# Optimization experiments

Measured on AMD Instinct MI355X. Metric: run time of the kernel, lower is better.

## Reference

```python
import jax, jax.numpy as jnp
import numpy as np
from jax import lax

AB = 2            # activation quant bits (args.ab)
BN_EPS = 1e-4


def binarize(w):
    # DoReFa 1-bit weight: sign(w) with straight-through estimator
    wb = jnp.where(w >= 0, 1.0, -1.0).astype(w.dtype)
    return w + lax.stop_gradient(wb - w)


def quantize(x, bits):
    # uniform quantization of x in [0,1] to `bits` bits, STE backward
    n = float(2 ** bits - 1)
    q = jnp.round(x * n) / n
    return x + lax.stop_gradient(q - x)


def conv(x, w, pad, b=None):
    y = lax.conv_general_dilated(x, w, window_strides=(1, 1),
                                 padding=[(pad, pad), (pad, pad)],
                                 dimension_numbers=('NCHW', 'OIHW', 'NCHW'))
    if b is not None:
        y = y + b[None, :, None, None]
    return y


def maxpool2(x):
    return lax.reduce_window(x, -jnp.inf, lax.max, (1, 1, 2, 2), (1, 1, 2, 2), 'VALID')


def bn(x, gamma, beta, mean, var):
    inv = gamma * lax.rsqrt(var + BN_EPS)
    return (x - mean[None, :, None, None]) * inv[None, :, None, None] + beta[None, :, None, None]


def setup_inputs() -> dict:
    key = jax.random.key(0)
    ks = jax.random.split(key, 16)
    s = lambda k, shape, sc=0.1: jax.random.normal(k, shape, dtype=jnp.float32) * sc
    return {
        'x': jax.random.uniform(ks[0], (4096, 1, 28, 28), dtype=jnp.float32),
        'w1': s(ks[1], (64, 1, 3, 3)), 'b1': s(ks[2], (64,)),
        'w2': s(ks[3], (64, 64, 3, 3)),
        'g1': 1.0 + s(ks[4], (64,)), 'be1': s(ks[5], (64,)),
        'm1': s(ks[6], (64,)), 'v1': 0.5 + jax.random.uniform(ks[7], (64,), dtype=jnp.float32),
        'w3': s(ks[8], (64, 64, 3, 3)),
        'g2': 1.0 + s(ks[9], (64,)), 'be2': s(ks[10], (64,)),
        'm2': s(ks[11], (64,)), 'v2': 0.5 + jax.random.uniform(ks[12], (64,), dtype=jnp.float32),
        'fw1': s(ks[13], (512, 1600)), 'fb1': s(ks[13], (512,)),
        'fw2': s(ks[14], (10, 512)), 'fb2': s(ks[15], (10,)),
    }


def reference(x, w1, b1, w2, g1, be1, m1, v1, w3, g2, be2, m2, v2, fw1, fb1, fw2, fb2):
    x = x.reshape(-1, 1, 28, 28)
    # features
    h = conv(x, binarize(w1), pad=1, b=b1)                 # [B,64,28,28]
    h = maxpool2(h)                                        # [B,64,14,14]
    h = quantize(jnp.clip(h, 0.0, 1.0), AB)
    h = conv(h, binarize(w2), pad=1)                       # [B,64,14,14]
    h = bn(h, g1, be1, m1, v1)
    h = quantize(jnp.clip(h, 0.0, 1.0), AB)
    h = maxpool2(h)                                        # [B,64,7,7]
    h = conv(h, binarize(w3), pad=0)                       # [B,64,5,5]
    h = bn(h, g2, be2, m2, v2)
    h = quantize(jnp.clip(h, 0.0, 1.0), AB)
    # NCHW -> NHWC -> flatten (matches permute((0,2,3,1)) + view)
    h = jnp.transpose(h, (0, 2, 3, 1)).reshape(-1, 64 * 5 * 5)
    # classifier
    h = h @ binarize(fw1).T + fb1                          # [B,512]
    h = h @ fw2.T + fb2                                    # [B,10]
    return jax.nn.log_softmax(h, axis=-1)
```

## Files before the change

kernel.cpp:

```cpp
#include <hip/hip_runtime.h>

#define DEV __device__ __forceinline__

typedef int v4i __attribute__((ext_vector_type(4)));
typedef short v8s __attribute__((ext_vector_type(8)));
typedef float v4f __attribute__((ext_vector_type(4)));
typedef unsigned long long u64;

DEV unsigned int quant3(float y3) {
    return (unsigned int)(int)rintf(fminf(fmaxf(y3, 0.f), 3.f));
}

DEV int imax(int a, int b) { return a > b ? a : b; }
DEV int imin(int a, int b) { return a < b ? a : b; }

DEV unsigned int f2bf(float x) {
    union { float f; unsigned u; } v; v.f = x;
    unsigned r = v.u + 0x7fffu + ((v.u >> 16) & 1u);
    return r >> 16;
}
DEV float bf2f(unsigned int b) {
    union { unsigned u; float f; } v; v.u = b << 16;
    return v.f;
}
#define SPLIT3(v, H, M, L)                        \
    unsigned int H = f2bf(v);                     \
    float r1_##H = (v) - bf2f(H);                 \
    unsigned int M = f2bf(r1_##H);                \
    unsigned int L = f2bf(r1_##H - bf2f(M));

DEV v8s mk_v8s(u64 a, u64 b) {
    union { u64 q[2]; v8s s; } u; u.q[0] = a; u.q[1] = b; return u.s;
}

DEV int chpos(int c) { return (c & 15) * 4 + (c >> 4); }

__global__ __launch_bounds__(256) void k_signs(
    const float* __restrict__ w2, const float* __restrict__ w3,
    const float* __restrict__ fw1,
    char* __restrict__ w2p, char* __restrict__ w3p, char* __restrict__ fw1s) {
    int i = blockIdx.x * 256 + threadIdx.x;
    if (i < 36864) {
        int co = i / 576, r = i - co * 576;
        int ci = r / 9, t = r - ci * 9;
        int p = chpos(ci);
        int off = t * 4096 + (p >> 4) * 1024 + co * 16 + (p & 15);
        w2p[off] = (w2[i] >= 0.f) ? 1 : -1;
        w3p[off] = (w3[i] >= 0.f) ? 1 : -1;
    }
    if (i < 819200) {
        int o = i / 1600, r2 = i - o * 1600;
        int pix = r2 >> 6, ch = r2 & 63;
        fw1s[o * 1600 + pix * 64 + chpos(ch)] = (fw1[i] >= 0.f) ? 1 : -1;
    }
}

__global__ __launch_bounds__(256, 4) void k_conv1_mfma(
    const float* __restrict__ x, const float* __restrict__ w1f,
    const float* __restrict__ b1, unsigned char* __restrict__ a1) {
    __shared__ u64 simg[960];
    __shared__ float sxf[960];
    int b = blockIdx.x, tid = threadIdx.x;
    for (int i = tid; i < 960; i += 256) {
        int y = i >> 5, xc = i & 31;
        float v = 0.f;
        if (y >= 1 && y <= 28 && xc >= 1 && xc <= 28)
            v = x[(size_t)b * 784 + (y - 1) * 28 + (xc - 1)];
        sxf[i] = v;
        SPLIT3(v, h, m, lo);
        simg[i] = (u64)(h | (m << 16)) | ((u64)lo << 32);
    }
    int l = tid & 63, lr = l & 15, lg = l >> 4, w = tid >> 6;
    int t0 = lg * 2, t1 = t0 + 1;
    int ky0 = (t0 * 21846) >> 16, kx0 = t0 - ky0 * 3;
    int ky1 = (t1 * 21846) >> 16, kx1 = t1 - ky1 * 3;
    int dt0 = (ky0 * 32 + kx0) * 8, dt1 = (ky1 * 32 + kx1) * 8;
    v8s bf[4];
    float s8[4], b3[4];
#pragma unroll
    for (int nt = 0; nt < 4; ++nt) {
        const float* wr = w1f + (nt * 16 + lr) * 9;
        unsigned sa = (wr[t0] >= 0.f) ? 0x3F80u : 0xBF80u;
        unsigned sb = (wr[t1] >= 0.f) ? 0x3F80u : 0xBF80u;
        union { unsigned d[4]; v8s s; } u;
        u.d[0] = sa | (sa << 16); u.d[1] = sa;
        u.d[2] = sb | (sb << 16); u.d[3] = sb;
        bf[nt] = u.s;
        s8[nt] = (wr[8] >= 0.f) ? 1.f : -1.f;
        b3[nt] = 3.f * b1[nt * 16 + lr];
    }
    __syncthreads();

    const unsigned char* sib = (const unsigned char*)simg;
    unsigned char* outb = a1 + (size_t)b * 12544;
    for (int mt = w; mt < 49; mt += 4) {
        int s = mt * 4 + (lr >> 2);
        int qy = (s * 4682) >> 16;
        int qx = s - qy * 14;
        int cy = 2 * qy + ((lr >> 1) & 1);
        int cx = 2 * qx + (lr & 1);
        int base = (cy * 32 + cx) * 8;
        u64 qa = *(const u64*)(sib + base + dt0);
        u64 qb = *(const u64*)(sib + base + dt1);
        v8s af = mk_v8s(qa, qb);
        v4f a0 = {0.f, 0.f, 0.f, 0.f}, a1v = {0.f, 0.f, 0.f, 0.f};
        v4f a2v = {0.f, 0.f, 0.f, 0.f}, a3v = {0.f, 0.f, 0.f, 0.f};
        a0  = __builtin_amdgcn_mfma_f32_16x16x32_bf16(af, bf[0], a0, 0, 0, 0);
        a1v = __builtin_amdgcn_mfma_f32_16x16x32_bf16(af, bf[1], a1v, 0, 0, 0);
        a2v = __builtin_amdgcn_mfma_f32_16x16x32_bf16(af, bf[2], a2v, 0, 0, 0);
        a3v = __builtin_amdgcn_mfma_f32_16x16x32_bf16(af, bf[3], a3v, 0, 0, 0);
        int q = mt * 4 + lg;
        int Qy = (q * 4682) >> 16;
        int Qx = q - Qy * 14;
        const float* xr = &sxf[(2 * Qy + 2) * 32 + (2 * Qx + 2)];
        float x8_0 = xr[0], x8_1 = xr[1], x8_2 = xr[32], x8_3 = xr[33];
        unsigned dw;
        {
            float m0 = fmaxf(fmaxf(fmaf(s8[0], x8_0, a0[0]),  fmaf(s8[0], x8_1, a0[1])),
                             fmaxf(fmaf(s8[0], x8_2, a0[2]),  fmaf(s8[0], x8_3, a0[3])));
            float m1 = fmaxf(fmaxf(fmaf(s8[1], x8_0, a1v[0]), fmaf(s8[1], x8_1, a1v[1])),
                             fmaxf(fmaf(s8[1], x8_2, a1v[2]), fmaf(s8[1], x8_3, a1v[3])));
            float m2 = fmaxf(fmaxf(fmaf(s8[2], x8_0, a2v[0]), fmaf(s8[2], x8_1, a2v[1])),
                             fmaxf(fmaf(s8[2], x8_2, a2v[2]), fmaf(s8[2], x8_3, a2v[3])));
            float m3 = fmaxf(fmaxf(fmaf(s8[3], x8_0, a3v[0]), fmaf(s8[3], x8_1, a3v[1])),
                             fmaxf(fmaf(s8[3], x8_2, a3v[2]), fmaf(s8[3], x8_3, a3v[3])));
            dw  = quant3(fmaf(m0, 3.f, b3[0]));
            dw |= quant3(fmaf(m1, 3.f, b3[1])) << 8;
            dw |= quant3(fmaf(m2, 3.f, b3[2])) << 16;
            dw |= quant3(fmaf(m3, 3.f, b3[3])) << 24;
        }
        *(unsigned*)(outb + q * 64 + lr * 4) = dw;
    }
}

__global__ __launch_bounds__(256, 3) void k_conv2_mfma(
    const unsigned char* __restrict__ a1, const char* __restrict__ w2p,
    const float* __restrict__ g1, const float* __restrict__ be1,
    const float* __restrict__ m1, const float* __restrict__ v1,
    unsigned char* __restrict__ a2) {
    __shared__ unsigned char sa[16384];
    __shared__ char sw[36864];
    int b = blockIdx.x, tid = threadIdx.x;
    if (tid < 240) {
        int ck = tid & 3, e = tid >> 2;
        int py, px;
        if (e < 16)      { py = 0;      px = e; }
        else if (e < 32) { py = 15;     px = e - 16; }
        else if (e < 46) { py = e - 31; px = 0; }
        else             { py = e - 45; px = 15; }
        *(uint4*)(sa + ck * 4096 + (py * 16 + px) * 16) = make_uint4(0, 0, 0, 0);
    }
    {
        const uint4* src = (const uint4*)(a1 + (size_t)b * 12544);
        for (int i = tid; i < 784; i += 256) {
            int ck = i / 196, pixel = i - ck * 196;
            int py = pixel / 14, px = pixel - py * 14;
            *(uint4*)(sa + ck * 4096 + ((py + 1) * 16 + px + 1) * 16) =
                src[pixel * 4 + ck];
        }
        const uint4* wsrc = (const uint4*)w2p;
        uint4* wdst = (uint4*)sw;
        for (int i = tid; i < 2304; i += 256) wdst[i] = wsrc[i];
    }
    __syncthreads();

    int w = tid >> 6, l = tid & 63;
    int lr = l & 15, lg = l >> 4;
    int abase[4], mts[4];
#pragma unroll
    for (int j = 0; j < 4; ++j) {
        int mt = w + 4 * j;
        mts[j] = mt;
        int s = mt * 4 + (lr >> 2);
        if (s > 48) s = 48;
        int qy = s / 7, qx = s - qy * 7;
        int ty = 2 * qy + ((lr >> 1) & 1);
        int tx = 2 * qx + (lr & 1);
        abase[j] = lg * 4096 + (ty * 16 + tx) * 16;
    }
    v4i acc[4][4] = {};
#pragma unroll
    for (int t = 0; t < 9; ++t) {
        int ky = t / 3, kx = t - ky * 3;
        int boff = t * 4096 + lg * 1024 + lr * 16;
        v4i bfw[4];
#pragma unroll
        for (int nt = 0; nt < 4; ++nt)
            bfw[nt] = *(const v4i*)(sw + boff + nt * 256);
        int aoff = (ky * 16 + kx) * 16;
#pragma unroll
        for (int j = 0; j < 4; ++j) {
            if (mts[j] < 13) {
                v4i af = *(const v4i*)(sa + abase[j] + aoff);
#pragma unroll
                for (int nt = 0; nt < 4; ++nt)
                    acc[j][nt] = __builtin_amdgcn_mfma_i32_16x16x64_i8(
                        af, bfw[nt], acc[j][nt], 0, 0, 0);
            }
        }
    }

    float sc4[4], of4[4];
#pragma unroll
    for (int nt = 0; nt < 4; ++nt) {
        int ch = nt * 16 + lr;
        float si = g1[ch] * rsqrtf(v1[ch] + 1e-4f);
        sc4[nt] = si;
        of4[nt] = 3.f * (be1[ch] - m1[ch] * si);
    }
#pragma unroll
    for (int j = 0; j < 4; ++j) {
        int q = mts[j] * 4 + lg;
        if (q < 49) {
            unsigned dw = 0;
#pragma unroll
            for (int nt = 0; nt < 4; ++nt) {
                int mx = imax(imax(acc[j][nt][0], acc[j][nt][1]),
                              imax(acc[j][nt][2], acc[j][nt][3]));
                int mn = imin(imin(acc[j][nt][0], acc[j][nt][1]),
                              imin(acc[j][nt][2], acc[j][nt][3]));
                float sc = sc4[nt];
                int v = (sc >= 0.f) ? mx : mn;
                dw |= quant3(fmaf((float)v, sc, of4[nt])) << (8 * nt);
            }
            *(unsigned*)(a2 + (size_t)b * 3136 + q * 64 + lr * 4) = dw;
        }
    }
}

__global__ __launch_bounds__(256, 2) void k_conv3_mfma(
    const unsigned char* __restrict__ a2, const char* __restrict__ w3p,
    const float* __restrict__ g2, const float* __restrict__ be2,
    const float* __restrict__ m2, const float* __restrict__ v2,
    unsigned char* __restrict__ a3) {
    __shared__ unsigned char sa[4 * 3136];
    __shared__ char sw[36864];
    __shared__ unsigned char so[4 * 2560];
    int b0 = blockIdx.x * 4, tid = threadIdx.x;
    {
        const uint4* src = (const uint4*)(a2 + (size_t)b0 * 3136);
        for (int i = tid; i < 784; i += 256) {
            int img = i / 196, r = i - img * 196;
            int ck = r / 49, pixel = r - ck * 49;
            *(uint4*)(sa + img * 3136 + ck * 784 + pixel * 16) =
                src[img * 196 + pixel * 4 + ck];
        }
        const uint4* wsrc = (const uint4*)w3p;
        uint4* wdst = (uint4*)sw;
        for (int i = tid; i < 2304; i += 256) wdst[i] = wsrc[i];
    }
    __syncthreads();

    int w = tid >> 6, l = tid & 63;
    int lr = l & 15, lg = l >> 4;
    const unsigned char* sai = sa + w * 3136;
    int abase[2];
#pragma unroll
    for (int mt = 0; mt < 2; ++mt) {
        int p = mt * 16 + lr;
        if (p > 24) p = 24;
        int oy = p / 5, ox = p - oy * 5;
        abase[mt] = lg * 784 + (oy * 7 + ox) * 16;
    }
    v4i acc[2][4] = {};
#pragma unroll
    for (int t = 0; t < 9; ++t) {
        int ky = t / 3, kx = t - ky * 3;
        int boff = t * 4096 + lg * 1024 + lr * 16;
        v4i bfw[4];
#pragma unroll
        for (int nt = 0; nt < 4; ++nt)
            bfw[nt] = *(const v4i*)(sw + boff + nt * 256);
        int aoff = (ky * 7 + kx) * 16;
#pragma unroll
        for (int mt = 0; mt < 2; ++mt) {
            v4i af = *(const v4i*)(sai + abase[mt] + aoff);
#pragma unroll
            for (int nt = 0; nt < 4; ++nt)
                acc[mt][nt] = __builtin_amdgcn_mfma_i32_16x16x64_i8(
                    af, bfw[nt], acc[mt][nt], 0, 0, 0);
        }
    }

    float sc4[4], of4[4];
#pragma unroll
    for (int nt = 0; nt < 4; ++nt) {
        int ch = nt * 16 + lr;
        float si = g2[ch] * rsqrtf(v2[ch] + 1e-4f);
        sc4[nt] = si;
        of4[nt] = 3.f * (be2[ch] - m2[ch] * si);
    }
    unsigned char* soi = so + w * 2560;
#pragma unroll
    for (int mt = 0; mt < 2; ++mt)
#pragma unroll
        for (int r = 0; r < 4; ++r) {
            int pixel = mt * 16 + lg * 4 + r;
            unsigned dw = 0;
#pragma unroll
            for (int nt = 0; nt < 4; ++nt)
                dw |= quant3(fmaf((float)acc[mt][nt][r], sc4[nt], of4[nt])) << (8 * nt);
            *(unsigned*)(soi + pixel * 80 + lr * 4) = dw;
        }
    __syncthreads();
    for (int idx = tid; idx < 400; idx += 256) {
        int img = idx / 100, r = idx - img * 100;
        int p = r >> 2, c0 = r & 3;
        *(uint4*)(a3 + (size_t)(b0 + img) * 1600 + r * 16) =
            *(const uint4*)(so + img * 2560 + p * 80 + c0 * 16);
    }
}

__global__ __launch_bounds__(256) void k_fc1_mfma(
    const unsigned char* __restrict__ a3, const char* __restrict__ fw1s,
    const float* __restrict__ fb1, float* __restrict__ h1) {
    __shared__ unsigned char sA[64 * 80];
    __shared__ unsigned char sB[64 * 80];
    __shared__ float sbias[64];
    int bb = (blockIdx.x >> 3) * 64;
    int ob = (blockIdx.x & 7) * 64;
    int tid = threadIdx.x;
    int row = tid >> 2, seg = tid & 3;
    if (tid < 64) sbias[tid] = fb1[ob + tid];
    const unsigned char* Ag = a3 + (size_t)(bb + row) * 1600 + seg * 16;
    const char* Bg = fw1s + (size_t)(ob + row) * 1600 + seg * 16;
    uint4 av = *(const uint4*)Ag;
    uint4 bv = *(const uint4*)Bg;

    int w = tid >> 6, l = tid & 63;
    int wm = w >> 1, wn = w & 1;
    int lr = l & 15, lg = l >> 4;
    const unsigned char* sAr = sA + (wm * 32 + lr) * 80 + lg * 16;
    const unsigned char* sBr = sB + (wn * 32 + lr) * 80 + lg * 16;
    v4i acc[2][2] = {};

    for (int k0 = 0; k0 < 1600; k0 += 64) {
        *(uint4*)(sA + row * 80 + seg * 16) = av;
        *(uint4*)(sB + row * 80 + seg * 16) = bv;
        __syncthreads();
        if (k0 < 1536) {
            av = *(const uint4*)(Ag + k0 + 64);
            bv = *(const uint4*)(Bg + k0 + 64);
        }
        v4i af0 = *(const v4i*)(sAr);
        v4i af1 = *(const v4i*)(sAr + 16 * 80);
        v4i bf0 = *(const v4i*)(sBr);
        v4i bf1 = *(const v4i*)(sBr + 16 * 80);
        acc[0][0] = __builtin_amdgcn_mfma_i32_16x16x64_i8(af0, bf0, acc[0][0], 0, 0, 0);
        acc[0][1] = __builtin_amdgcn_mfma_i32_16x16x64_i8(af0, bf1, acc[0][1], 0, 0, 0);
        acc[1][0] = __builtin_amdgcn_mfma_i32_16x16x64_i8(af1, bf0, acc[1][0], 0, 0, 0);
        acc[1][1] = __builtin_amdgcn_mfma_i32_16x16x64_i8(af1, bf1, acc[1][1], 0, 0, 0);
        __syncthreads();
    }

    const float inv3 = 1.f / 3.f;
#pragma unroll
    for (int mt = 0; mt < 2; ++mt)
#pragma unroll
        for (int nt = 0; nt < 2; ++nt) {
            int gcol = ob + wn * 32 + nt * 16 + lr;
            float bias = sbias[wn * 32 + nt * 16 + lr];
#pragma unroll
            for (int r = 0; r < 4; ++r) {
                int grow = bb + wm * 32 + mt * 16 + lg * 4 + r;
                h1[(size_t)grow * 512 + gcol] = (float)acc[mt][nt][r] * inv3 + bias;
            }
        }
}

__global__ __launch_bounds__(256) void k_fc2(
    const float* __restrict__ h1, const float* __restrict__ fw2,
    const float* __restrict__ fb2, float* __restrict__ out) {
    __shared__ float sw[5120];
    __shared__ float sb[16];
    int tid = threadIdx.x;
    for (int i = tid; i < 5120; i += 256) sw[i] = fw2[i];
    if (tid < 10) sb[tid] = fb2[tid];
    __syncthreads();

    int wv = tid >> 6, lane = tid & 63;
    int b = blockIdx.x * 4 + wv;
    const float* hr = h1 + (size_t)b * 512;
    float p[10];
#pragma unroll
    for (int o = 0; o < 10; ++o) p[o] = 0.f;
    for (int k = lane; k < 512; k += 64) {
        float hv = hr[k];
#pragma unroll
        for (int o = 0; o < 10; ++o) p[o] += hv * sw[o * 512 + k];
    }
#pragma unroll
    for (int o = 0; o < 10; ++o) {
#pragma unroll
        for (int off = 32; off > 0; off >>= 1) p[o] += __shfl_xor(p[o], off, 64);
        p[o] += sb[o];
    }
    float mx = p[0];
#pragma unroll
    for (int o = 1; o < 10; ++o) mx = fmaxf(mx, p[o]);
    float se = 0.f;
#pragma unroll
    for (int o = 0; o < 10; ++o) se += expf(p[o] - mx);
    float lse = logf(se) + mx;
    float myv = 0.f;
#pragma unroll
    for (int o = 0; o < 10; ++o) myv = (lane == o) ? p[o] : myv;
    if (lane < 10) out[(size_t)b * 10 + lane] = myv - lse;
}

extern "C" void kernel_launch(void* const* d_in, const int* in_sizes, int n_in,
                              void* d_out, int out_size, void* d_ws, size_t ws_size,
                              hipStream_t stream) {
    const float* x   = (const float*)d_in[0];
    const float* w1  = (const float*)d_in[1];
    const float* b1  = (const float*)d_in[2];
    const float* w2  = (const float*)d_in[3];
    const float* g1  = (const float*)d_in[4];
    const float* be1 = (const float*)d_in[5];
    const float* m1  = (const float*)d_in[6];
    const float* v1  = (const float*)d_in[7];
    const float* w3  = (const float*)d_in[8];
    const float* g2  = (const float*)d_in[9];
    const float* be2 = (const float*)d_in[10];
    const float* m2  = (const float*)d_in[11];
    const float* v2  = (const float*)d_in[12];
    const float* fw1 = (const float*)d_in[13];
    const float* fb1 = (const float*)d_in[14];
    const float* fw2 = (const float*)d_in[15];
    const float* fb2 = (const float*)d_in[16];
    float* out = (float*)d_out;

    char* ws = (char*)d_ws;
    char* w2p  = ws;
    char* w3p  = ws + 36864;
    char* fw1s = ws + 73728;
    unsigned char* a1 = (unsigned char*)(ws + 892928);
    unsigned char* a2 = a1 + 51380224;
    unsigned char* a3 = a2 + 12845056;
    float* h1 = (float*)(void*)a1;

    k_signs<<<3200, 256, 0, stream>>>(w2, w3, fw1, w2p, w3p, fw1s);
    k_conv1_mfma<<<4096, 256, 0, stream>>>(x, w1, b1, a1);
    k_conv2_mfma<<<4096, 256, 0, stream>>>(a1, w2p, g1, be1, m1, v1, a2);
    k_conv3_mfma<<<1024, 256, 0, stream>>>(a2, w3p, g2, be2, m2, v2, a3);
    k_fc1_mfma<<<512, 256, 0, stream>>>(a3, fw1s, fb1, h1);
    k_fc2<<<1024, 256, 0, stream>>>(h1, fw2, fb2, out);
}
```

Baseline: 113.3 us.

## Fuse conv1 and conv2 into one kernel keeping activations in LDS

Merges the conv1+pool+quantize kernel with the conv2 kernel so each block writes its quantized 14x14x64 activation tile straight into shared memory instead of round-tripping through a 51 MB global buffer. The shared-memory chunk stride is padded (CKS) to reduce bank conflicts. Shared memory per block grows and the occupancy hint drops to 2 blocks per SM, which may reduce latency hiding. The h1 buffer is relocated since a1 no longer exists.

```diff
diff --git a/kernel.cpp b/kernel.cpp
--- a/kernel.cpp
+++ b/kernel.cpp
@@ -34,6 +34,8 @@
 }
 
 DEV int chpos(int c) { return (c & 15) * 4 + (c >> 4); }
+
+#define CKS 4160
 
 __global__ __launch_bounds__(256) void k_signs(
     const float* __restrict__ w2, const float* __restrict__ w3,
@@ -55,12 +57,18 @@
     }
 }
 
-__global__ __launch_bounds__(256, 4) void k_conv1_mfma(
+__global__ __launch_bounds__(256, 2) void k_conv12(
     const float* __restrict__ x, const float* __restrict__ w1f,
-    const float* __restrict__ b1, unsigned char* __restrict__ a1) {
+    const float* __restrict__ b1, const char* __restrict__ w2p,
+    const float* __restrict__ g1, const float* __restrict__ be1,
+    const float* __restrict__ m1, const float* __restrict__ v1,
+    unsigned char* __restrict__ a2) {
     __shared__ u64 simg[960];
     __shared__ float sxf[960];
+    __shared__ unsigned char sa[4 * CKS];
+    __shared__ char sw[36864];
     int b = blockIdx.x, tid = threadIdx.x;
+
     for (int i = tid; i < 960; i += 256) {
         int y = i >> 5, xc = i & 31;
         float v = 0.f;
@@ -70,6 +78,23 @@
         SPLIT3(v, h, m, lo);
         simg[i] = (u64)(h | (m << 16)) | ((u64)lo << 32);
     }
+    {
+        const uint4* wsrc = (const uint4*)w2p;
+        for (int i = tid; i < 2304; i += 256) {
+            int t = i >> 8, r = i & 255;
+            *(uint4*)(sw + t * 4096 + r * 16) = wsrc[i];
+        }
+    }
+    if (tid < 240) {
+        int ck = tid & 3, e = tid >> 2;
+        int py, px;
+        if (e < 16)      { py = 0;      px = e; }
+        else if (e < 32) { py = 15;     px = e - 16; }
+        else if (e < 46) { py = e - 31; px = 0; }
+        else             { py = e - 45; px = 15; }
+        *(uint4*)(sa + ck * CKS + (py * 16 + px) * 16) = make_uint4(0, 0, 0, 0);
+    }
+
     int l = tid & 63, lr = l & 15, lg = l >> 4, w = tid >> 6;
     int t0 = lg * 2, t1 = t0 + 1;
     int ky0 = (t0 * 21846) >> 16, kx0 = t0 - ky0 * 3;
@@ -80,92 +105,69 @@
 #pragma unroll
     for (int nt = 0; nt < 4; ++nt) {
         const float* wr = w1f + (nt * 16 + lr) * 9;
-        unsigned sa = (wr[t0] >= 0.f) ? 0x3F80u : 0xBF80u;
-        unsigned sb = (wr[t1] >= 0.f) ? 0x3F80u : 0xBF80u;
+        unsigned sa_ = (wr[t0] >= 0.f) ? 0x3F80u : 0xBF80u;
+        unsigned sb_ = (wr[t1] >= 0.f) ? 0x3F80u : 0xBF80u;
         union { unsigned d[4]; v8s s; } u;
-        u.d[0] = sa | (sa << 16); u.d[1] = sa;
-        u.d[2] = sb | (sb << 16); u.d[3] = sb;
+        u.d[0] = sa_ | (sa_ << 16); u.d[1] = sa_;
+        u.d[2] = sb_ | (sb_ << 16); u.d[3] = sb_;
         bf[nt] = u.s;
         s8[nt] = (wr[8] >= 0.f) ? 1.f : -1.f;
         b3[nt] = 3.f * b1[nt * 16 + lr];
     }
+    float sc4[4], of4[4];
+#pragma unroll
+    for (int nt = 0; nt < 4; ++nt) {
+        int ch = nt * 16 + lr;
+        float si = g1[ch] * rsqrtf(v1[ch] + 1e-4f);
+        sc4[nt] = si;
+        of4[nt] = 3.f * (be1[ch] - m1[ch] * si);
+    }
     __syncthreads();
 
-    const unsigned char* sib = (const unsigned char*)simg;
-    unsigned char* outb = a1 + (size_t)b * 12544;
-    for (int mt = w; mt < 49; mt += 4) {
-        int s = mt * 4 + (lr >> 2);
-        int qy = (s * 4682) >> 16;
-        int qx = s - qy * 14;
-        int cy = 2 * qy + ((lr >> 1) & 1);
-        int cx = 2 * qx + (lr & 1);
-        int base = (cy * 32 + cx) * 8;
-        u64 qa = *(const u64*)(sib + base + dt0);
-        u64 qb = *(const u64*)(sib + base + dt1);
-        v8s af = mk_v8s(qa, qb);
-        v4f a0 = {0.f, 0.f, 0.f, 0.f}, a1v = {0.f, 0.f, 0.f, 0.f};
-        v4f a2v = {0.f, 0.f, 0.f, 0.f}, a3v = {0.f, 0.f, 0.f, 0.f};
-        a0  = __builtin_amdgcn_mfma_f32_16x16x32_bf16(af, bf[0], a0, 0, 0, 0);
-        a1v = __builtin_amdgcn_mfma_f32_16x16x32_bf16(af, bf[1], a1v, 0, 0, 0);
-        a2v = __builtin_amdgcn_mfma_f32_16x16x32_bf16(af, bf[2], a2v, 0, 0, 0);
-        a3v = __builtin_amdgcn_mfma_f32_16x16x32_bf16(af, bf[3], a3v, 0, 0, 0);
-        int q = mt * 4 + lg;
-        int Qy = (q * 4682) >> 16;
-        int Qx = q - Qy * 14;
-        const float* xr = &sxf[(2 * Qy + 2) * 32 + (2 * Qx + 2)];
-        float x8_0 = xr[0], x8_1 = xr[1], x8_2 = xr[32], x8_3 = xr[33];
-        unsigned dw;
-        {
-            float m0 = fmaxf(fmaxf(fmaf(s8[0], x8_0, a0[0]),  fmaf(s8[0], x8_1, a0[1])),
-                             fmaxf(fmaf(s8[0], x8_2, a0[2]),  fmaf(s8[0], x8_3, a0[3])));
-            float m1 = fmaxf(fmaxf(fmaf(s8[1], x8_0, a1v[0]), fmaf(s8[1], x8_1, a1v[1])),
-                             fmaxf(fmaf(s8[1], x8_2, a1v[2]), fmaf(s8[1], x8_3, a1v[3])));
-            float m2 = fmaxf(fmaxf(fmaf(s8[2], x8_0, a2v[0]), fmaf(s8[2], x8_1, a2v[1])),
-                             fmaxf(fmaf(s8[2], x8_2, a2v[2]), fmaf(s8[2], x8_3, a2v[3])));
-            float m3 = fmaxf(fmaxf(fmaf(s8[3], x8_0, a3v[0]), fmaf(s8[3], x8_1, a3v[1])),
-                             fmaxf(fmaf(s8[3], x8_2, a3v[2]), fmaf(s8[3], x8_3, a3v[3])));
-            dw  = quant3(fmaf(m0, 3.f, b3[0]));
-            dw |= quant3(fmaf(m1, 3.f, b3[1])) << 8;
-            dw |= quant3(fmaf(m2, 3.f, b3[2])) << 16;
-            dw |= quant3(fmaf(m3, 3.f, b3[3])) << 24;
-        }
-        *(unsigned*)(outb + q * 64 + lr * 4) = dw;
-    }
-}
-
-__global__ __launch_bounds__(256, 3) void k_conv2_mfma(
-    const unsigned char* __restrict__ a1, const char* __restrict__ w2p,
-    const float* __restrict__ g1, const float* __restrict__ be1,
-    const float* __restrict__ m1, const float* __restrict__ v1,
-    unsigned char* __restrict__ a2) {
-    __shared__ unsigned char sa[16384];
-    __shared__ char sw[36864];
-    int b = blockIdx.x, tid = threadIdx.x;
-    if (tid < 240) {
-        int ck = tid & 3, e = tid >> 2;
-        int py, px;
-        if (e < 16)      { py = 0;      px = e; }
-        else if (e < 32) { py = 15;     px = e - 16; }
-        else if (e < 46) { py = e - 31; px = 0; }
-        else             { py = e - 45; px = 15; }
-        *(uint4*)(sa + ck * 4096 + (py * 16 + px) * 16) = make_uint4(0, 0, 0, 0);
-    }
     {
-        const uint4* src = (const uint4*)(a1 + (size_t)b * 12544);
-        for (int i = tid; i < 784; i += 256) {
-            int ck = i / 196, pixel = i - ck * 196;
-            int py = pixel / 14, px = pixel - py * 14;
-            *(uint4*)(sa + ck * 4096 + ((py + 1) * 16 + px + 1) * 16) =
-                src[pixel * 4 + ck];
-        }
-        const uint4* wsrc = (const uint4*)w2p;
-        uint4* wdst = (uint4*)sw;
-        for (int i = tid; i < 2304; i += 256) wdst[i] = wsrc[i];
+        const unsigned char* sib = (const unsigned char*)simg;
+        for (int mt = w; mt < 49; mt += 4) {
+            int s = mt * 4 + (lr >> 2);
+            int qy = (s * 4682) >> 16;
+            int qx = s - qy * 14;
+            int cy = 2 * qy + ((lr >> 1) & 1);
+            int cx = 2 * qx + (lr & 1);
+            int base = (cy * 32 + cx) * 8;
+            u64 qa = *(const u64*)(sib + base + dt0);
+            u64 qb = *(const u64*)(sib + base + dt1);
+            v8s af = mk_v8s(qa, qb);
+            v4f a0 = {0.f, 0.f, 0.f, 0.f}, a1v = {0.f, 0.f, 0.f, 0.f};
+            v4f a2v = {0.f, 0.f, 0.f, 0.f}, a3v = {0.f, 0.f, 0.f, 0.f};
+            a0  = __builtin_amdgcn_mfma_f32_16x16x32_bf16(af, bf[0], a0, 0, 0, 0);
+            a1v = __builtin_amdgcn_mfma_f32_16x16x32_bf16(af, bf[1], a1v, 0, 0, 0);
+            a2v = __builtin_amdgcn_mfma_f32_16x16x32_bf16(af, bf[2], a2v, 0, 0, 0);
+            a3v = __builtin_amdgcn_mfma_f32_16x16x32_bf16(af, bf[3], a3v, 0, 0, 0);
+            int q = mt * 4 + lg;
+            int Qy = (q * 4682) >> 16;
+            int Qx = q - Qy * 14;
+            const float* xr = &sxf[(2 * Qy + 2) * 32 + (2 * Qx + 2)];
+            float x8_0 = xr[0], x8_1 = xr[1], x8_2 = xr[32], x8_3 = xr[33];
+            unsigned dw;
+            {
+                float m0 = fmaxf(fmaxf(fmaf(s8[0], x8_0, a0[0]),  fmaf(s8[0], x8_1, a0[1])),
+                                 fmaxf(fmaf(s8[0], x8_2, a0[2]),  fmaf(s8[0], x8_3, a0[3])));
+                float m1 = fmaxf(fmaxf(fmaf(s8[1], x8_0, a1v[0]), fmaf(s8[1], x8_1, a1v[1])),
+                                 fmaxf(fmaf(s8[1], x8_2, a1v[2]), fmaf(s8[1], x8_3, a1v[3])));
+                float m2 = fmaxf(fmaxf(fmaf(s8[2], x8_0, a2v[0]), fmaf(s8[2], x8_1, a2v[1])),
+                                 fmaxf(fmaf(s8[2], x8_2, a2v[2]), fmaf(s8[2], x8_3, a2v[3])));
+                float m3 = fmaxf(fmaxf(fmaf(s8[3], x8_0, a3v[0]), fmaf(s8[3], x8_1, a3v[1])),
+                                 fmaxf(fmaf(s8[3], x8_2, a3v[2]), fmaf(s8[3], x8_3, a3v[3])));
+                dw  = quant3(fmaf(m0, 3.f, b3[0]));
+                dw |= quant3(fmaf(m1, 3.f, b3[1])) << 8;
+                dw |= quant3(fmaf(m2, 3.f, b3[2])) << 16;
+                dw |= quant3(fmaf(m3, 3.f, b3[3])) << 24;
+            }
+            *(unsigned*)(sa + (lr >> 2) * CKS + ((Qy + 1) * 16 + (Qx + 1)) * 16
+                         + (lr & 3) * 4) = dw;
+        }
     }
     __syncthreads();
 
-    int w = tid >> 6, l = tid & 63;
-    int lr = l & 15, lg = l >> 4;
     int abase[4], mts[4];
 #pragma unroll
     for (int j = 0; j < 4; ++j) {
@@ -176,7 +178,7 @@
         int qy = s / 7, qx = s - qy * 7;
         int ty = 2 * qy + ((lr >> 1) & 1);
         int tx = 2 * qx + (lr & 1);
-        abase[j] = lg * 4096 + (ty * 16 + tx) * 16;
+        abase[j] = lg * CKS + (ty * 16 + tx) * 16;
     }
     v4i acc[4][4] = {};
 #pragma unroll
@@ -198,15 +200,6 @@
                         af, bfw[nt], acc[j][nt], 0, 0, 0);
             }
         }
-    }
-
-    float sc4[4], of4[4];
-#pragma unroll
-    for (int nt = 0; nt < 4; ++nt) {
-        int ch = nt * 16 + lr;
-        float si = g1[ch] * rsqrtf(v1[ch] + 1e-4f);
-        sc4[nt] = si;
-        of4[nt] = 3.f * (be1[ch] - m1[ch] * si);
     }
 #pragma unroll
     for (int j = 0; j < 4; ++j) {
@@ -434,14 +427,12 @@
     char* w2p  = ws;
     char* w3p  = ws + 36864;
     char* fw1s = ws + 73728;
-    unsigned char* a1 = (unsigned char*)(ws + 892928);
-    unsigned char* a2 = a1 + 51380224;
+    unsigned char* a2 = (unsigned char*)(ws + 892928);
     unsigned char* a3 = a2 + 12845056;
-    float* h1 = (float*)(void*)a1;
+    float* h1 = (float*)(void*)(a3 + 6553600);
 
     k_signs<<<3200, 256, 0, stream>>>(w2, w3, fw1, w2p, w3p, fw1s);
-    k_conv1_mfma<<<4096, 256, 0, stream>>>(x, w1, b1, a1);
-    k_conv2_mfma<<<4096, 256, 0, stream>>>(a1, w2p, g1, be1, m1, v1, a2);
+    k_conv12<<<4096, 256, 0, stream>>>(x, w1, b1, w2p, g1, be1, m1, v1, a2);
     k_conv3_mfma<<<1024, 256, 0, stream>>>(a2, w3p, g2, be2, m2, v2, a3);
     k_fc1_mfma<<<512, 256, 0, stream>>>(a3, fw1s, fb1, h1);
     k_fc2<<<1024, 256, 0, stream>>>(h1, fw2, fb2, out);
```

After: 126.2 us. +11.4%, slower.
